# Performance work log

Measured on AMD Instinct MI355X. Metric: run time of the kernel, lower is better.

## Reference

```python
import jax, jax.numpy as jnp
import numpy as np
from jax import lax

# ---- static config (from init_kwargs / input_specs) ----
B, NB, C, F = 16, 8192, 3, 64   # batches, points-per-batch, coord dim, feat dim
RATIO, K = 0.125, 16
M = int(RATIO * NB)


def setup_inputs() -> dict:
    key = jax.random.key(0)
    kx, kp = jax.random.split(key)
    x = jax.random.normal(kx, (B * NB, F), dtype=jnp.float32)
    pos = jax.random.normal(kp, (B * NB, C), dtype=jnp.float32)
    batch = (jnp.arange(B * NB, dtype=jnp.int32) // NB).astype(jnp.int32)
    return {"x": x, "pos": pos, "batch": batch}


def _fps_single(pos_b):
    """Sequential farthest point sampling on (NB, C), deterministic start at 0.
    Returns (M,) int32 indices into pos_b."""
    n = pos_b.shape[0]

    def step(carry, _):
        min_d2, last = carry
        d2 = jnp.sum((pos_b - pos_b[last]) ** 2, axis=-1)   # (NB,)
        min_d2 = jnp.minimum(min_d2, d2)
        nxt = jnp.argmax(min_d2).astype(jnp.int32)
        return (min_d2, nxt), last

    init = (jnp.full((n,), jnp.finfo(pos_b.dtype).max, dtype=pos_b.dtype),
            jnp.int32(0))
    _, idx = lax.scan(step, init, None, length=M)
    return idx  # (M,)


def reference(x, pos, batch):
    # batch ids are block-constant (batch[i] = i // NB), so per-batch views are
    # simple reshapes -- same semantics as torch_cluster's batched fps/knn.
    pos_b = pos.reshape(B, NB, C)

    # --- farthest point sampling per batch ---
    fps_idx = jax.vmap(_fps_single)(pos_b)                            # (B, M)
    centroids = jnp.take_along_axis(pos_b, fps_idx[..., None], axis=1)  # (B, M, C)

    # --- k-NN: squared distances centroids -> all points of same batch ---
    d2 = (jnp.sum(centroids ** 2, axis=-1)[..., None]
          - 2.0 * jnp.einsum('bmc,bnc->bmn', centroids, pos_b)
          + jnp.sum(pos_b ** 2, axis=-1)[:, None, :])                 # (B, M, NB)
    _, nn_idx = lax.top_k(-d2, K)                                     # (B, M, K)

    # gather neighbor coordinates (== pos[groups_idx[1]])
    groups = jax.vmap(lambda p, i: p[i])(pos_b, nn_idx.reshape(B, M * K))  # (B, M*K, C)

    return centroids.reshape(B * M, C), groups.reshape(B * M * K, C)
```

## Files before the change

### kernel.cpp

```cpp
#include <hip/hip_runtime.h>
#include <float.h>
#include <math.h>

#define B_   16
#define NB_  8192
#define M_   1024
#define K_   16


#define FPS_T 512
#define PPT   16

__global__ __launch_bounds__(FPS_T, 2) void fps_kernel(const float* __restrict__ pos,
                                                       float* __restrict__ cent)
{
    #pragma clang fp contract(off)
    const int b = blockIdx.x;
    const int t = threadIdx.x;
    const float* pb = pos + (size_t)b * NB_ * 3;
    float* cb = cent + (size_t)b * M_ * 3;

    __shared__ float sx[NB_], sy[NB_], sz[NB_];
    __shared__ unsigned long long wkey[2][FPS_T / 64];

    float px[PPT], py[PPT], pz[PPT], md[PPT];
    #pragma unroll
    for (int j = 0; j < PPT; ++j) {
        const int i = t * PPT + j;
        const float* s = pb + (size_t)i * 3;
        float x = s[0], y = s[1], z = s[2];
        px[j] = x; py[j] = y; pz[j] = z;
        sx[i] = x; sy[i] = y; sz[i] = z;
        md[j] = FLT_MAX;
    }
    __syncthreads();

    float lx = pb[0], ly = pb[1], lz = pb[2];
    float c0x = 0.f, c0y = 0.f, c0z = 0.f, c1x = 0.f, c1y = 0.f, c1z = 0.f;

    for (int m = 0; m < M_; ++m) {
        if (t == (m >> 1)) {
            if (m & 1) { c1x = lx; c1y = ly; c1z = lz; }
            else       { c0x = lx; c0y = ly; c0z = lz; }
        }
        if (m == M_ - 1) break;

        float bestv = -1.0f;
        int   besti = 0;
        #pragma unroll
        for (int j = 0; j < PPT; ++j) {
            float dx = px[j] - lx;
            float dy = py[j] - ly;
            float dz = pz[j] - lz;
            float d2 = (dx*dx + dy*dy) + dz*dz;
            float mj = fminf(md[j], d2);
            md[j] = mj;
            bool g = mj > bestv;
            besti = g ? (t*PPT + j) : besti;
            bestv = g ? mj : bestv;
        }

        float v = bestv;
        {
            int vi;
            vi = __builtin_amdgcn_update_dpp(__float_as_int(v), __float_as_int(v), 0xB1,  0xF, 0xF, false);
            v = fmaxf(v, __int_as_float(vi));
            vi = __builtin_amdgcn_update_dpp(__float_as_int(v), __float_as_int(v), 0x4E,  0xF, 0xF, false);
            v = fmaxf(v, __int_as_float(vi));
            vi = __builtin_amdgcn_update_dpp(__float_as_int(v), __float_as_int(v), 0x141, 0xF, 0xF, false);
            v = fmaxf(v, __int_as_float(vi));
            vi = __builtin_amdgcn_update_dpp(__float_as_int(v), __float_as_int(v), 0x140, 0xF, 0xF, false);
            v = fmaxf(v, __int_as_float(vi));
            vi = __builtin_amdgcn_update_dpp(__float_as_int(v), __float_as_int(v), 0x142, 0xF, 0xF, false);
            v = fmaxf(v, __int_as_float(vi));
            vi = __builtin_amdgcn_update_dpp(__float_as_int(v), __float_as_int(v), 0x143, 0xF, 0xF, false);
            v = fmaxf(v, __int_as_float(vi));
        }
        const float wmax = __int_as_float(__builtin_amdgcn_readlane(__float_as_int(v), 63));
        unsigned long long mk = __ballot(bestv == wmax);
        const int wl = (int)__ffsll(mk) - 1;
        const int widx = __builtin_amdgcn_readlane(besti, wl);

        const int par = m & 1;
        if ((t & 63) == 0)
            wkey[par][t >> 6] = ((unsigned long long)__float_as_uint(wmax) << 32) |
                                (unsigned int)(~widx);
        __syncthreads();

        unsigned long long kk = wkey[par][0];
        #pragma unroll
        for (int w = 1; w < FPS_T/64; ++w) {
            unsigned long long e = wkey[par][w];
            kk = (e > kk) ? e : kk;
        }
        const int best = (int)(~(unsigned int)kk);

        lx = sx[best]; ly = sy[best]; lz = sz[best];
    }

    {
        float* o0 = cb + (size_t)(2*t) * 3;
        o0[0] = c0x; o0[1] = c0y; o0[2] = c0z;
        o0[3] = c1x; o0[4] = c1y; o0[5] = c1z;
    }
}

#define KNN_T   256
#define CHUNK   1024
#define GRP     8
#define BCAP    16
#define BSTRIDE 17

__device__ __forceinline__ void topk_insert(float d2, int pi, float val[16], int idx[16])
{
    int r = 0;
    #pragma unroll
    for (int j = 0; j < 16; ++j) r += (val[j] <= d2) ? 1 : 0;
    #pragma unroll
    for (int j = 15; j >= 1; --j) {
        bool sh = (j > r);
        val[j] = sh ? val[j-1] : val[j];
        idx[j] = sh ? idx[j-1] : idx[j];
    }
    #pragma unroll
    for (int j = 0; j < 16; ++j) {
        bool pl = (j == r);
        val[j] = pl ? d2 : val[j];
        idx[j] = pl ? pi : idx[j];
    }
}

__global__ __launch_bounds__(KNN_T, 2) void knn_kernel(const float* __restrict__ pos,
    const float* __restrict__ cent, float* __restrict__ groups,
    unsigned long long* __restrict__ partials, int nsplit)
{
    #pragma clang fp contract(off)
    __shared__ float4 spts[CHUNK];
    __shared__ unsigned long long sbuf[KNN_T * BSTRIDE];

    const int wg = blockIdx.x;
    const int t  = threadIdx.x;
    const int per_b = 4 * nsplit;
    const int b  = wg / per_b;
    const int r  = wg % per_b;
    const int cg = r / nsplit;
    const int sp = r % nsplit;
    const int span  = NB_ / nsplit;
    const int pbase = sp * span;
    const int nchunks = span / CHUNK;

    const float* pb = pos + (size_t)b * NB_ * 3;
    const int mg = b * M_ + cg * KNN_T + t;
    const float cx = cent[(size_t)mg*3+0];
    const float cy = cent[(size_t)mg*3+1];
    const float cz = cent[(size_t)mg*3+2];
    const float cn2 = (cx*cx + cy*cy) + cz*cz;

    float val[16]; int idx[16];
    #pragma unroll
    for (int j = 0; j < 16; ++j) { val[j] = FLT_MAX; idx[j] = 0; }
    float tau = FLT_MAX;
    int cnt = 0;
    unsigned long long* mybuf = sbuf + t * BSTRIDE;

    for (int c = 0; c < nchunks; ++c) {
        const int ps = pbase + c * CHUNK;
        __syncthreads();
        for (int p = t; p < CHUNK; p += KNN_T) {
            const float* s = pb + (size_t)(ps + p) * 3;
            float x = s[0], y = s[1], z = s[2];
            float pn2 = (x*x + y*y) + z*z;
            spts[p] = make_float4(x, y, z, pn2);
        }
        __syncthreads();

        for (int p0 = 0; p0 < CHUNK; p0 += GRP) {
            if (__any(cnt > BCAP - GRP)) {
                int n = cnt; cnt = 0;
                for (int i = 0; i < n; ++i) {
                    unsigned long long e = mybuf[i];
                    float d = __uint_as_float((unsigned int)(e >> 32));
                    int pi  = (int)(e & 0xFFFFFFFFu);
                    if (d < val[15]) topk_insert(d, pi, val, idx);
                }
                tau = val[15];
            }
            float4 q[GRP];
            #pragma unroll
            for (int i = 0; i < GRP; ++i) q[i] = spts[p0 + i];
            float d2v[GRP];
            #pragma unroll
            for (int i = 0; i < GRP; ++i) {
                float dot = __builtin_fmaf(cz, q[i].z,
                            __builtin_fmaf(cy, q[i].y, cx * q[i].x));
                d2v[i] = (cn2 - 2.0f*dot) + q[i].w;
            }
            #pragma unroll
            for (int i = 0; i < GRP; ++i) {
                if (d2v[i] < tau) {
                    mybuf[cnt] = ((unsigned long long)__float_as_uint(d2v[i]) << 32) |
                                 (unsigned int)(ps + p0 + i);
                    ++cnt;
                }
            }
        }
    }
    {
        int n = cnt;
        for (int i = 0; i < n; ++i) {
            unsigned long long e = mybuf[i];
            float d = __uint_as_float((unsigned int)(e >> 32));
            int pi  = (int)(e & 0xFFFFFFFFu);
            if (d < val[15]) topk_insert(d, pi, val, idx);
        }
    }

    if (nsplit > 1) {
        unsigned long long* o = partials + ((size_t)mg * nsplit + sp) * 16;
        #pragma unroll
        for (int kq = 0; kq < 16; ++kq)
            o[kq] = ((unsigned long long)__float_as_uint(val[kq]) << 32) | (unsigned int)idx[kq];
    } else {
        float* g = groups + (size_t)mg * K_ * 3;
        #pragma unroll
        for (int kq = 0; kq < 16; ++kq) {
            const float* s = pb + (size_t)idx[kq] * 3;
            g[kq*3+0] = s[0]; g[kq*3+1] = s[1]; g[kq*3+2] = s[2];
        }
    }
}

__global__ __launch_bounds__(256, 2) void knn_merge(const float* __restrict__ pos,
    const unsigned long long* __restrict__ partials, float* __restrict__ groups,
    int nsplit)
{
    const int mg = blockIdx.x * 256 + threadIdx.x;
    const int b  = mg >> 10;
    const float* pb = pos + (size_t)b * NB_ * 3;

    float val[16]; int idx[16];
    #pragma unroll
    for (int j = 0; j < 16; ++j) { val[j] = FLT_MAX; idx[j] = 0; }
    for (int sp = 0; sp < nsplit; ++sp) {
        const unsigned long long* l = partials + ((size_t)mg * nsplit + sp) * 16;
        #pragma unroll
        for (int kq = 0; kq < 16; ++kq) {
            unsigned long long e = l[kq];
            float d = __uint_as_float((unsigned int)(e >> 32));
            int pi  = (int)(e & 0xFFFFFFFFu);
            if (d < val[15]) topk_insert(d, pi, val, idx);
        }
    }
    float* g = groups + (size_t)mg * K_ * 3;
    #pragma unroll
    for (int kq = 0; kq < 16; ++kq) {
        const float* s = pb + (size_t)idx[kq] * 3;
        g[kq*3+0] = s[0]; g[kq*3+1] = s[1]; g[kq*3+2] = s[2];
    }
}

extern "C" void kernel_launch(void* const* d_in, const int* in_sizes, int n_in,
                              void* d_out, int out_size, void* d_ws, size_t ws_size,
                              hipStream_t stream)
{
    (void)in_sizes; (void)n_in; (void)out_size;
    const float* pos = (const float*)d_in[1];
    float* out    = (float*)d_out;
    float* cent   = out;
    float* groups = out + (size_t)B_ * M_ * 3;

    fps_kernel<<<B_, FPS_T, 0, stream>>>(pos, cent);

    const size_t lst = (size_t)B_ * M_ * 16 * sizeof(unsigned long long);
    int nsplit = (ws_size >= 8*lst) ? 8 : (ws_size >= 4*lst) ? 4 : (ws_size >= 2*lst) ? 2 : 1;

    knn_kernel<<<B_ * 4 * nsplit, KNN_T, 0, stream>>>(pos, cent, groups,
                                                      (unsigned long long*)d_ws, nsplit);
    if (nsplit > 1)
        knn_merge<<<(B_ * M_) / 256, 256, 0, stream>>>(pos,
                                                      (const unsigned long long*)d_ws,
                                                      groups, nsplit);
}
```

Baseline: 1.411 ms.

## Vectorize FPS distance update with packed float2 and defer argmax index search

The FPS inner loop now runs on two-wide float vectors, which lets the compiler emit packed FP32 math, and tracks only the running max instead of a per-point index. The argmax index is recovered afterwards: the winning wave and lane rescan their registers for the matching value, which costs a second block barrier per iteration. Points are staged once in shared memory as float4 so a centroid can be fetched with a single load. The goal is to shorten the per-iteration critical path of the sequential 1024-step loop, at the price of an extra sync and a serial rescan in one lane.

```diff
diff --git a/kernel.cpp b/kernel.cpp
--- a/kernel.cpp
+++ b/kernel.cpp
@@ -7,6 +7,8 @@
 #define M_   1024
 #define K_   16
 
+
+typedef float v2f __attribute__((ext_vector_type(2)));
 
 #define FPS_T 512
 #define PPT   16
@@ -20,47 +22,52 @@
     const float* pb = pos + (size_t)b * NB_ * 3;
     float* cb = cent + (size_t)b * M_ * 3;
 
-    __shared__ float sx[NB_], sy[NB_], sz[NB_];
-    __shared__ unsigned long long wkey[2][FPS_T / 64];
-
-    float px[PPT], py[PPT], pz[PPT], md[PPT];
-    #pragma unroll
-    for (int j = 0; j < PPT; ++j) {
-        const int i = t * PPT + j;
-        const float* s = pb + (size_t)i * 3;
-        float x = s[0], y = s[1], z = s[2];
-        px[j] = x; py[j] = y; pz[j] = z;
-        sx[i] = x; sy[i] = y; sz[i] = z;
-        md[j] = FLT_MAX;
+    __shared__ float4 spts[NB_];
+    __shared__ float  swmax[2][FPS_T / 64];
+    __shared__ int    swidx[2];
+
+    for (int p = t; p < NB_; p += FPS_T) {
+        const float* s = pb + (size_t)p * 3;
+        spts[p] = make_float4(s[0], s[1], s[2], 0.0f);
     }
     __syncthreads();
 
+    v2f px2[PPT/2], py2[PPT/2], pz2[PPT/2], md2[PPT/2];
+    #pragma unroll
+    for (int jj = 0; jj < PPT/2; ++jj) {
+        float4 a = spts[t*PPT + 2*jj];
+        float4 c = spts[t*PPT + 2*jj + 1];
+        px2[jj] = (v2f){a.x, c.x};
+        py2[jj] = (v2f){a.y, c.y};
+        pz2[jj] = (v2f){a.z, c.z};
+        md2[jj] = (v2f){FLT_MAX, FLT_MAX};
+    }
+
     float lx = pb[0], ly = pb[1], lz = pb[2];
-    float c0x = 0.f, c0y = 0.f, c0z = 0.f, c1x = 0.f, c1y = 0.f, c1z = 0.f;
+    float c0x=0.0f,c0y=0.0f,c0z=0.0f,c1x=0.0f,c1y=0.0f,c1z=0.0f;
 
     for (int m = 0; m < M_; ++m) {
         if (t == (m >> 1)) {
-            if (m & 1) { c1x = lx; c1y = ly; c1z = lz; }
-            else       { c0x = lx; c0y = ly; c0z = lz; }
+            if (m & 1) { c1x=lx; c1y=ly; c1z=lz; }
+            else       { c0x=lx; c0y=ly; c0z=lz; }
         }
         if (m == M_ - 1) break;
 
-        float bestv = -1.0f;
-        int   besti = 0;
+        const v2f lxv = {lx,lx}, lyv = {ly,ly}, lzv = {lz,lz};
+        v2f bmax2 = {-1.0f, -1.0f};
         #pragma unroll
-        for (int j = 0; j < PPT; ++j) {
-            float dx = px[j] - lx;
-            float dy = py[j] - ly;
-            float dz = pz[j] - lz;
-            float d2 = (dx*dx + dy*dy) + dz*dz;
-            float mj = fminf(md[j], d2);
-            md[j] = mj;
-            bool g = mj > bestv;
-            besti = g ? (t*PPT + j) : besti;
-            bestv = g ? mj : bestv;
-        }
-
-        float v = bestv;
+        for (int jj = 0; jj < PPT/2; ++jj) {
+            v2f dx = px2[jj] - lxv;
+            v2f dy = py2[jj] - lyv;
+            v2f dz = pz2[jj] - lzv;
+            v2f d2 = (dx*dx + dy*dy) + dz*dz;
+            v2f mj = __builtin_elementwise_min(md2[jj], d2);
+            md2[jj] = mj;
+            bmax2 = __builtin_elementwise_max(bmax2, mj);
+        }
+        float bm = fmaxf(bmax2.x, bmax2.y);
+
+        float v = bm;
         {
             int vi;
             vi = __builtin_amdgcn_update_dpp(__float_as_int(v), __float_as_int(v), 0xB1,  0xF, 0xF, false);
@@ -76,33 +83,44 @@
             vi = __builtin_amdgcn_update_dpp(__float_as_int(v), __float_as_int(v), 0x143, 0xF, 0xF, false);
             v = fmaxf(v, __int_as_float(vi));
         }
-        const float wmax = __int_as_float(__builtin_amdgcn_readlane(__float_as_int(v), 63));
-        unsigned long long mk = __ballot(bestv == wmax);
-        const int wl = (int)__ffsll(mk) - 1;
-        const int widx = __builtin_amdgcn_readlane(besti, wl);
+        const float wv = __int_as_float(__builtin_amdgcn_readlane(__float_as_int(v), 63));
 
         const int par = m & 1;
-        if ((t & 63) == 0)
-            wkey[par][t >> 6] = ((unsigned long long)__float_as_uint(wmax) << 32) |
-                                (unsigned int)(~widx);
+        if ((t & 63) == 0) swmax[par][t >> 6] = wv;
         __syncthreads();
 
-        unsigned long long kk = wkey[par][0];
-        #pragma unroll
-        for (int w = 1; w < FPS_T/64; ++w) {
-            unsigned long long e = wkey[par][w];
-            kk = (e > kk) ? e : kk;
-        }
-        const int best = (int)(~(unsigned int)kk);
-
-        lx = sx[best]; ly = sy[best]; lz = sz[best];
-    }
-
-    {
-        float* o0 = cb + (size_t)(2*t) * 3;
-        o0[0] = c0x; o0[1] = c0y; o0[2] = c0z;
-        o0[3] = c1x; o0[4] = c1y; o0[5] = c1z;
-    }
+        const float w0 = swmax[par][0], w1 = swmax[par][1], w2 = swmax[par][2], w3 = swmax[par][3];
+        const float w4 = swmax[par][4], w5 = swmax[par][5], w6 = swmax[par][6], w7 = swmax[par][7];
+        const float gmax = fmaxf(fmaxf(fmaxf(w0,w1), fmaxf(w2,w3)),
+                                 fmaxf(fmaxf(w4,w5), fmaxf(w6,w7)));
+        int lw = 7;
+        lw = (w6 == gmax) ? 6 : lw;
+        lw = (w5 == gmax) ? 5 : lw;
+        lw = (w4 == gmax) ? 4 : lw;
+        lw = (w3 == gmax) ? 3 : lw;
+        lw = (w2 == gmax) ? 2 : lw;
+        lw = (w1 == gmax) ? 1 : lw;
+        lw = (w0 == gmax) ? 0 : lw;
+
+        unsigned long long mk = __ballot(bm == gmax);
+        if ((t >> 6) == lw && (t & 63) == (int)__ffsll(mk) - 1) {
+            int idx = t * PPT;
+            bool found = false;
+            #pragma unroll
+            for (int jj = 0; jj < PPT/2; ++jj) {
+                if (!found && md2[jj].x == gmax) { idx = t*PPT + 2*jj;     found = true; }
+                if (!found && md2[jj].y == gmax) { idx = t*PPT + 2*jj + 1; found = true; }
+            }
+            swidx[par] = idx;
+        }
+        __syncthreads();
+
+        const float4 c = spts[swidx[par]];
+        lx = c.x; ly = c.y; lz = c.z;
+    }
+
+    float* o0 = cb + (size_t)(2*t) * 3;
+    o0[0]=c0x; o0[1]=c0y; o0[2]=c0z; o0[3]=c1x; o0[4]=c1y; o0[5]=c1z;
 }
 
 #define KNN_T   256
```

New measurement: 1.520 ms. 1.08x slower.
